# Optimization experiments

Hardware: AMD Instinct MI355X
Metric: run time of the kernel (lower is better)

Reference implementation:

```python
import jax, jax.numpy as jnp
import numpy as np

WINDOW_SIZE = 11
SIGMA = 1.5
MAX_VAL = 1.0


def _gaussian_kernel2d(ws: int, sigma: float) -> jnp.ndarray:
    # matches kornia gaussian_t: x = arange(ws) - ws//2, normalized 1D, outer product
    x = jnp.arange(ws, dtype=jnp.float32) - ws // 2
    g = jnp.exp(-(x * x) / (2.0 * sigma * sigma))
    g = g / g.sum()
    return jnp.outer(g, g)  # (ws, ws)


def _filter2d(x: jnp.ndarray, kernel: jnp.ndarray) -> jnp.ndarray:
    # depthwise 'same' conv with reflect padding, matching kornia filter2d
    B, C, H, W = x.shape
    kh, kw = kernel.shape
    pad_h = ((kh - 1) // 2, (kh - 1) - (kh - 1) // 2)
    pad_w = ((kw - 1) // 2, (kw - 1) - (kw - 1) // 2)
    xp = jnp.pad(x, ((0, 0), (0, 0), pad_h, pad_w), mode='reflect')
    k = jnp.broadcast_to(kernel[None, None], (C, 1, kh, kw)).astype(x.dtype)
    return jax.lax.conv_general_dilated(
        xp, k, window_strides=(1, 1), padding='VALID',
        dimension_numbers=('NCHW', 'OIHW', 'NCHW'), feature_group_count=C)


def setup_inputs() -> dict:
    key = jax.random.key(0)
    k1, k2 = jax.random.split(key)
    img1 = jax.random.uniform(k1, (16, 3, 512, 512), dtype=jnp.float32)
    img2 = jax.random.uniform(k2, (16, 3, 512, 512), dtype=jnp.float32)
    kernel = _gaussian_kernel2d(WINDOW_SIZE, SIGMA)  # fixed gaussian window (11,11)
    return {"img1": img1, "img2": img2, "kernel": kernel}


def reference(img1, img2, kernel):
    C1 = (0.01 * MAX_VAL) ** 2
    C2 = (0.03 * MAX_VAL) ** 2
    mu1 = _filter2d(img1, kernel)
    mu2 = _filter2d(img2, kernel)
    mu1_sq = mu1 * mu1
    mu2_sq = mu2 * mu2
    mu1_mu2 = mu1 * mu2
    sigma1_sq = _filter2d(img1 * img1, kernel) - mu1_sq
    sigma2_sq = _filter2d(img2 * img2, kernel) - mu2_sq
    sigma12 = _filter2d(img1 * img2, kernel) - mu1_mu2
    num = (2.0 * mu1_mu2 + C1) * (2.0 * sigma12 + C2)
    den = (mu1_sq + mu2_sq + C1) * (sigma1_sq + sigma2_sq + C2)
    return num / den  # (B, C, H, W) SSIM map ('same' padding -> no crop)
```

## Files before the change

### kernel.cpp

```cpp
#include <hip/hip_runtime.h>

namespace {

typedef __attribute__((ext_vector_type(2))) float f32x2;
typedef __attribute__((ext_vector_type(4))) float f32x4;

constexpr int Hd = 512, Wd = 512;
constexpr int TH = 32;
constexpr int R  = 4;
constexpr int NCH = TH / R;
constexpr int RAD = 5, WS = 11;
constexpr int SPAN = 131;
constexpr int RSTR = 4 * SPAN;
constexpr float C1c = 1e-4f;
constexpr float C2c = 9e-4f;

__device__ __forceinline__ float rcp_fast(float x) { return __builtin_amdgcn_rcpf(x); }
__device__ __forceinline__ float sgpr_f(float x) {
    return __int_as_float(__builtin_amdgcn_readfirstlane(__float_as_int(x)));
}
__device__ __forceinline__ constexpr int sw(int e) { return (e & 3) * SPAN + (e >> 2); }


#define VPHASE(CH, PA, PB, BUF)                                         \
    _Pragma("unroll")                                                   \
    for (int i = 0; i < R; ++i) {                                       \
        const int o = (CH) * R + i;                                     \
        const int j = o + 2 * RAD;                                      \
        const float a = (PA)[i];                                        \
        const float b = (PB)[i];                                        \
        f32x2 sd; sd.x = a + b; sd.y = a - b;                           \
        const f32x2 qq = sd * sd;                                       \
        _Pragma("unroll")                                               \
        for (int k = 0; k < WS; ++k) {                                  \
            const int slot = (j - k) % WS;     \
            f32x2 w2; w2.x = g[k]; w2.y = g[k];                         \
            aM[slot] = __builtin_elementwise_fma(w2, sd, aM[slot]);     \
            aQ[slot] = __builtin_elementwise_fma(w2, qq, aQ[slot]);     \
        }                                                               \
        const int es = o % WS;                                          \
        f32x4 e;                                                        \
        e.x = aM[es].x; e.y = aM[es].y;                                 \
        e.z = aQ[es].x; e.w = aQ[es].y;                                 \
        (BUF)[i * RSTR + wmain] = e;                                    \
        if (whalo >= 0) (BUF)[i * RSTR + whalo] = e;                    \
        aM[es].x = 0.f; aM[es].y = 0.f;                                 \
        aQ[es].x = 0.f; aQ[es].y = 0.f;                                 \
    }

#define PREFETCH(CHUNK, PA, PB)                                         \
    _Pragma("unroll")                                                   \
    for (int i = 0; i < R; ++i) {                                       \
        int gr = row0 + RAD + (CHUNK) * R + i;                          \
        gr = (gr >= Hd) ? (2 * Hd - 2 - gr) : gr;                       \
        const long off = pbase + (long)gr * Wd + c;                     \
        (PA)[i] = img1[off];                                            \
        (PB)[i] = img2[off];                                            \
    }

__global__ __launch_bounds__(512, 4) void ssim_map_kernel(
    const float* __restrict__ img1,
    const float* __restrict__ img2,
    const float* __restrict__ kern,
    float* __restrict__ out)
{
    __shared__ __align__(16) f32x4 hb[2][R * RSTR];

    const int tid  = threadIdx.x;
    const int c    = tid;
    const int row0 = blockIdx.x * TH;
    const long pbase = (long)blockIdx.y * (long)(Hd * Wd);

    float g[WS];
    {
        float s = 0.f;
#pragma unroll
        for (int j = 0; j < WS; ++j) s += kern[RAD * WS + j];
        const float inv = 1.0f / s;
#pragma unroll
        for (int j = 0; j < WS; ++j) g[j] = sgpr_f(kern[RAD * WS + j] * inv);
    }

    const int wmain = sw(c + RAD);
    int whalo = -1;
    if (c >= 1 && c <= RAD) whalo = sw(RAD - c);
    else if (c >= Wd - 1 - RAD && c <= Wd - 2) whalo = sw(RAD + 1022 - c);

    f32x2 aM[WS];
    f32x2 aQ[WS];
#pragma unroll
    for (int i = 0; i < WS; ++i) {
        aM[i].x = 0.f; aM[i].y = 0.f;
        aQ[i].x = 0.f; aQ[i].y = 0.f;
    }

#pragma unroll
    for (int j = 0; j < 2 * RAD; ++j) {
        int gr = row0 - RAD + j;
        gr = (gr < 0) ? -gr : gr;
        gr = (gr >= Hd) ? (2 * Hd - 2 - gr) : gr;
        const long off = pbase + (long)gr * Wd + c;
        const float a = img1[off];
        const float b = img2[off];
        f32x2 sd; sd.x = a + b; sd.y = a - b;
        const f32x2 qq = sd * sd;
#pragma unroll
        for (int k = 0; k < WS; ++k) {
            if (k <= j) {
                const int slot = (j - k) % WS;
                f32x2 w2; w2.x = g[k]; w2.y = g[k];
                aM[slot] = __builtin_elementwise_fma(w2, sd, aM[slot]);
                aQ[slot] = __builtin_elementwise_fma(w2, qq, aQ[slot]);
            }
        }
    }

    float plaA[R], plbA[R], plaB[R], plbB[R];
    PREFETCH(0, plaA, plbA)
    PREFETCH(1, plaB, plbB)

    VPHASE(0, plaA, plbA, (&hb[0][0]))

    const int hr = tid >> 7;
    const int hu = tid & 127;

#pragma unroll
    for (int ch = 0; ch < NCH; ++ch) {
        __syncthreads();

        if (ch + 2 < NCH) {
            if ((ch & 1) == 0) { PREFETCH(ch + 2, plaA, plbA) }
            else               { PREFETCH(ch + 2, plaB, plbB) }
        }

        f32x2 hm[4], hq[4];
#pragma unroll
        for (int j = 0; j < 4; ++j) {
            hm[j].x = 0.f; hm[j].y = 0.f;
            hq[j].x = 0.f; hq[j].y = 0.f;
        }
        const f32x4* base = &hb[ch & 1][hr * RSTR + hu];
#pragma unroll
        for (int t = 0; t < 14; ++t) {
            const f32x4 ft = base[(t & 3) * SPAN + (t >> 2)];
            f32x2 fm; fm.x = ft.x; fm.y = ft.y;
            f32x2 fq; fq.x = ft.z; fq.y = ft.w;
#pragma unroll
            for (int j = 0; j < 4; ++j) {
                const int k = t - j;
                if (k >= 0 && k < WS) {
                    f32x2 w2; w2.x = g[k]; w2.y = g[k];
                    hm[j] = __builtin_elementwise_fma(w2, fm, hm[j]);
                    hq[j] = __builtin_elementwise_fma(w2, fq, hq[j]);
                }
            }
        }

        float rr[4];
#pragma unroll
        for (int j = 0; j < 4; ++j) {
            const f32x2 m = hm[j];
            const f32x2 q = hq[j];
            const f32x2 msq = m * m;
            const float t1 = msq.x - msq.y;
            const float t2 = msq.x + msq.y;
            const float q1 = q.x - q.y;
            const float q2 = q.x + q.y;
            const float num = fmaf(0.5f, t1, C1c) * fmaf(0.5f, q1 - t1, C2c);
            const float den = fmaf(0.5f, t2, C1c) * fmaf(0.5f, q2 - t2, C2c);
            rr[j] = num * rcp_fast(den);
        }
        f32x4 res; res.x = rr[0]; res.y = rr[1]; res.z = rr[2]; res.w = rr[3];
        f32x4* po = (f32x4*)&out[pbase + (long)(row0 + ch * R + hr) * Wd + 4 * hu];
        *po = res;

        if (ch + 1 < NCH) {
            if (((ch + 1) & 1) == 0) { VPHASE(ch + 1, plaA, plbA, (&hb[0][0])) }
            else                      { VPHASE(ch + 1, plaB, plbB, (&hb[1][0])) }
        }
    }
}

#undef VPHASE
#undef PREFETCH

}

extern "C" void kernel_launch(void* const* d_in, const int* in_sizes, int n_in,
                              void* d_out, int out_size, void* d_ws, size_t ws_size,
                              hipStream_t stream) {
    const float* img1 = (const float*)d_in[0];
    const float* img2 = (const float*)d_in[1];
    const float* kern = (const float*)d_in[2];
    float* outp = (float*)d_out;
    dim3 grid(Hd / TH, 48);
    ssim_map_kernel<<<grid, dim3(512), 0, stream>>>(img1, img2, kern, outp);
}
```

Measured before the change: 144.9 us.

## Single-buffer LDS staging with an extra barrier to raise occupancy to 6 blocks

The LDS staging buffer for vertically filtered values drops from double to single buffering. The vertical FMA results are kept in registers and written only after an added barrier, and launch bounds go from 4 to 6 blocks per SM. Halving LDS and capping registers is meant to allow more resident waves to hide global-load latency. The cost is a second __syncthreads per chunk, possible register spills under the tighter bound, and less overlap between the vertical and horizontal phases.

```diff
diff --git a/kernel.cpp b/kernel.cpp
--- a/kernel.cpp
+++ b/kernel.cpp
@@ -22,7 +22,7 @@
 __device__ __forceinline__ constexpr int sw(int e) { return (e & 3) * SPAN + (e >> 2); }
 
 
-#define VPHASE(CH, PA, PB, BUF)                                         \
+#define VFMA(CH, PA, PB)                                                \
     _Pragma("unroll")                                                   \
     for (int i = 0; i < R; ++i) {                                       \
         const int o = (CH) * R + i;                                     \
@@ -39,13 +39,17 @@
             aQ[slot] = __builtin_elementwise_fma(w2, qq, aQ[slot]);     \
         }                                                               \
         const int es = o % WS;                                          \
-        f32x4 e;                                                        \
-        e.x = aM[es].x; e.y = aM[es].y;                                 \
-        e.z = aQ[es].x; e.w = aQ[es].y;                                 \
-        (BUF)[i * RSTR + wmain] = e;                                    \
-        if (whalo >= 0) (BUF)[i * RSTR + whalo] = e;                    \
+        est[i].x = aM[es].x; est[i].y = aM[es].y;                       \
+        est[i].z = aQ[es].x; est[i].w = aQ[es].y;                       \
         aM[es].x = 0.f; aM[es].y = 0.f;                                 \
         aQ[es].x = 0.f; aQ[es].y = 0.f;                                 \
+    }
+
+#define VWRITE()                                                        \
+    _Pragma("unroll")                                                   \
+    for (int i = 0; i < R; ++i) {                                       \
+        hb[i * RSTR + wmain] = est[i];                                  \
+        if (whalo >= 0) hb[i * RSTR + whalo] = est[i];                  \
     }
 
 #define PREFETCH(CHUNK, PA, PB)                                         \
@@ -58,13 +62,13 @@
         (PB)[i] = img2[off];                                            \
     }
 
-__global__ __launch_bounds__(512, 4) void ssim_map_kernel(
+__global__ __launch_bounds__(512, 6) void ssim_map_kernel(
     const float* __restrict__ img1,
     const float* __restrict__ img2,
     const float* __restrict__ kern,
     float* __restrict__ out)
 {
-    __shared__ __align__(16) f32x4 hb[2][R * RSTR];
+    __shared__ __align__(16) f32x4 hb[R * RSTR];
 
     const int tid  = threadIdx.x;
     const int c    = tid;
@@ -119,7 +123,9 @@
     PREFETCH(0, plaA, plbA)
     PREFETCH(1, plaB, plbB)
 
-    VPHASE(0, plaA, plbA, (&hb[0][0]))
+    f32x4 est[R];
+    VFMA(0, plaA, plbA)
+    VWRITE()
 
     const int hr = tid >> 7;
     const int hu = tid & 127;
@@ -139,7 +145,7 @@
             hm[j].x = 0.f; hm[j].y = 0.f;
             hq[j].x = 0.f; hq[j].y = 0.f;
         }
-        const f32x4* base = &hb[ch & 1][hr * RSTR + hu];
+        const f32x4* base = &hb[hr * RSTR + hu];
 #pragma unroll
         for (int t = 0; t < 14; ++t) {
             const f32x4 ft = base[(t & 3) * SPAN + (t >> 2)];
@@ -175,13 +181,17 @@
         *po = res;
 
         if (ch + 1 < NCH) {
-            if (((ch + 1) & 1) == 0) { VPHASE(ch + 1, plaA, plbA, (&hb[0][0])) }
-            else                      { VPHASE(ch + 1, plaB, plbB, (&hb[1][0])) }
-        }
-    }
-}
-
-#undef VPHASE
+            if (((ch + 1) & 1) == 0) { VFMA(ch + 1, plaA, plbA) }
+            else                      { VFMA(ch + 1, plaB, plbB) }
+
+            __syncthreads();
+            VWRITE()
+        }
+    }
+}
+
+#undef VFMA
+#undef VWRITE
 #undef PREFETCH
 
 }
```

New measurement: 152.7 us. 1.05x slower.
